# Performance work log

Measured on AMD Instinct MI355X. Metric: run time of the kernel, lower is better.

Reference implementation:

```python
import jax, jax.numpy as jnp
import numpy as np
from jax import lax

B, H, W, C = 16, 32, 32, 256
HEADS = 8
HD = C // HEADS          # attention_head_dim = 32
KSZ = 3                  # conv_kernel_size
DIL = 2                  # dilation_rate
SCALE = HD ** -0.5


def setup_inputs() -> dict:
    key = jax.random.key(0)
    k0, k1, k2, k3 = jax.random.split(key, 4)
    return {
        "query": jax.random.normal(k0, (B, H, W, C), jnp.float32),
        "key_in": jax.random.normal(k1, (B, H, W, C), jnp.float32),
        "value": jax.random.normal(k2, (B, H, W, C), jnp.float32),
        # depthwise conv: kernel [kh, kw, in_ch/groups=1, out_ch=C], plus bias [C]
        "conv_kernel": jax.random.normal(k3, (KSZ, KSZ, 1, C), jnp.float32) * 0.05,
        "conv_bias": jnp.zeros((C,), jnp.float32),
    }


def _dwconv(x, kernel, bias):
    # depthwise dilated conv, padding SAME (Keras Conv2D groups=C)
    y = lax.conv_general_dilated(
        x, kernel,
        window_strides=(1, 1), padding="SAME",
        rhs_dilation=(DIL, DIL),
        dimension_numbers=("NHWC", "HWIO", "NHWC"),
        feature_group_count=C,
    )
    return y + bias


def _to_heads(x):
    # [B,H,W,C] -> [B, heads, S, head_dim]
    return x.reshape(B, H * W, HEADS, HD).transpose(0, 2, 1, 3)


def reference(query, key_in, value, conv_kernel, conv_bias):
    q = _to_heads(query)
    k = _to_heads(_dwconv(key_in, conv_kernel, conv_bias))
    v = _to_heads(_dwconv(value, conv_kernel, conv_bias))
    scores = jnp.einsum("bhqd,bhkd->bhqk", q, k) * SCALE  # [B,heads,S,S]
    attn = jax.nn.softmax(scores, axis=-1)
    out = jnp.einsum("bhqk,bhkd->bhqd", attn, v)          # [B,heads,S,hd]
    return out.transpose(0, 2, 1, 3).reshape(B, H, W, C)
```

## Files before the change

kernel.cpp:

```cpp
#include <hip/hip_runtime.h>

#define B_    16
#define HH    32
#define WW    32
#define CC    256
#define HEADS 8
#define HD    32
#define S_    1024
#define KT    128
#define NITER (S_ / KT)
#define QF    4
#define SCALE_L2E 0.25503486f

typedef unsigned short u16;
typedef unsigned int   u32;
typedef __attribute__((ext_vector_type(8))) short short8;
typedef __attribute__((ext_vector_type(4))) float f32x4;

__device__ __forceinline__ u16 f2bf(float f) {
    u32 x = __float_as_uint(f);
    return (u16)((x + 0x7fffu + ((x >> 16) & 1u)) >> 16);
}
__device__ __forceinline__ u32 pack2bf(float lo, float hi) {
    return (u32)f2bf(lo) | ((u32)f2bf(hi) << 16);
}

#define GLD_LDS16(gp, lp)                                                 \
    __builtin_amdgcn_global_load_lds(                                     \
        (const __attribute__((address_space(1))) void*)(gp),              \
        (__attribute__((address_space(3))) void*)(lp), 16, 0, 0)

__global__ __launch_bounds__(256, 5) void dw_conv_kernel(
    const float* __restrict__ key_in, const float* __restrict__ value,
    const float* __restrict__ ck, const float* __restrict__ cb,
    u16* __restrict__ Kws, u16* __restrict__ Vws)
{
    __shared__ float4 tile[2048];

    const int tid = threadIdx.x;
    const int blk = blockIdx.x;
    const int g  = blk & 7;
    const int yt = (blk >> 3) & 7;
    const int b  = (blk >> 6) & 15;
    const int t  = blk >> 10;
    const float4* __restrict__ src4 = (const float4*)(t ? value : key_in);
    const int y0 = yt * 4;

    {
        const int x  = (tid >> 3) & 31;
        const int cc = tid & 7;
        #pragma unroll
        for (int i = 0; i < 8; i++) {
            int yy = y0 - 2 + i;
            if (yy >= 0 && yy < HH) {
                const float4* gp = src4 +
                    ((((size_t)b * HH + yy) * WW + x) * 64 + g * 8 + cc);
                GLD_LDS16(gp, &tile[tid + i * 256]);
            }
        }
    }

    const int c = tid & 7;
    float4 w9[9];
    #pragma unroll
    for (int j = 0; j < 9; j++)
        w9[j] = *(const float4*)(ck + j * CC + g * 32 + c * 4);
    const float4 bias = *(const float4*)(cb + g * 32 + c * 4);

    __syncthreads();

    #pragma unroll
    for (int i = 0; i < 4; i++) {
        int o = tid + i * 256;
        int x = (o >> 3) & 31;
        const int ry = i;
        float4 acc = bias;
        #pragma unroll
        for (int kh = 0; kh < 3; kh++) {
            int yy = y0 + ry - 2 + 2 * kh;
            if (yy < 0 || yy >= HH) continue;
            #pragma unroll
            for (int kw = 0; kw < 3; kw++) {
                int xx = x - 2 + 2 * kw;
                if (xx < 0 || xx >= WW) continue;
                float4 v = tile[((ry + 2 * kh) * 32 + xx) * 8 + c];
                float4 w = w9[kh * 3 + kw];
                acc.x += w.x * v.x; acc.y += w.y * v.y;
                acc.z += w.z * v.z; acc.w += w.w * v.w;
            }
        }
        int spix = (y0 + ry) * WW + x;
        size_t off = (((size_t)(b * HEADS + g)) * S_ + spix) * HD + c * 4;
        if (t == 0)
            *(uint2*)&Kws[off] = make_uint2(pack2bf(acc.x * SCALE_L2E, acc.y * SCALE_L2E),
                                            pack2bf(acc.z * SCALE_L2E, acc.w * SCALE_L2E));
        else
            *(uint2*)&Vws[off] = make_uint2(pack2bf(acc.x, acc.y), pack2bf(acc.z, acc.w));
    }
}

__global__ __launch_bounds__(256, 2) void attn_kernel(
    const float* __restrict__ query,
    const u16* __restrict__ Kws, const u16* __restrict__ Vws,
    float* __restrict__ out)
{
    __shared__ __align__(16) u16 Vtlds[2][HD][KT + 8];

    const int tid  = threadIdx.x;
    const int lane = tid & 63;
    const int wv   = tid >> 6;
    const int q15  = lane & 15;
    const int quad = lane >> 4;

    const int blk = blockIdx.x;
    const int bh  = blk & 127;
    const int qt  = blk >> 7;
    const int b = bh >> 3, h = bh & 7;
    const int q0w = qt * 256 + wv * 64;

    short8 qf[QF];
    #pragma unroll
    for (int f = 0; f < QF; f++) {
        const float* qp = query + ((size_t)(b * S_ + q0w + f * 16 + q15)) * CC
                          + h * HD + quad * 8;
        float4 a = *(const float4*)(qp);
        float4 c = *(const float4*)(qp + 4);
        short8 v;
        v[0] = (short)f2bf(a.x); v[1] = (short)f2bf(a.y);
        v[2] = (short)f2bf(a.z); v[3] = (short)f2bf(a.w);
        v[4] = (short)f2bf(c.x); v[5] = (short)f2bf(c.y);
        v[6] = (short)f2bf(c.z); v[7] = (short)f2bf(c.w);
        qf[f] = v;
    }

    short8 ones;
    #pragma unroll
    for (int j = 0; j < 8; j++) ones[j] = (short)0x3F80;

    const u16* Kg = Kws + (size_t)bh * S_ * HD;
    const u16* Vg = Vws + (size_t)bh * S_ * HD;

    const int vg  = tid >> 3, vs4 = tid & 7;
    const int vc = vg >> 3, vw = vg & 7;
    const int vt2 = (vw >> 2) & 1, vqd = vw & 3;
    const int vpg = (vc << 5) | (vqd << 3) | (vt2 << 2);

    uint2 vr0, vr1, vr2, vr3;

    auto issue_v_loads = [&](int kt0) {
        const uint2* vsrc = (const uint2*)(Vg + (size_t)(kt0 + 4 * vg) * HD + 4 * vs4);
        vr0 = vsrc[0]; vr1 = vsrc[8]; vr2 = vsrc[16]; vr3 = vsrc[24];
    };
    auto write_lds = [&](int p) {
        u32 a, bb;
        a  = __builtin_amdgcn_perm(vr1.x, vr0.x, 0x05040100u);
        bb = __builtin_amdgcn_perm(vr3.x, vr2.x, 0x05040100u);
        *(uint2*)&Vtlds[p][4 * vs4 + 0][vpg] = make_uint2(a, bb);
        a  = __builtin_amdgcn_perm(vr1.x, vr0.x, 0x07060302u);
        bb = __builtin_amdgcn_perm(vr3.x, vr2.x, 0x07060302u);
        *(uint2*)&Vtlds[p][4 * vs4 + 1][vpg] = make_uint2(a, bb);
        a  = __builtin_amdgcn_perm(vr1.y, vr0.y, 0x05040100u);
        bb = __builtin_amdgcn_perm(vr3.y, vr2.y, 0x05040100u);
        *(uint2*)&Vtlds[p][4 * vs4 + 2][vpg] = make_uint2(a, bb);
        a  = __builtin_amdgcn_perm(vr1.y, vr0.y, 0x07060302u);
        bb = __builtin_amdgcn_perm(vr3.y, vr2.y, 0x07060302u);
        *(uint2*)&Vtlds[p][4 * vs4 + 3][vpg] = make_uint2(a, bb);
    };

    f32x4 Ot[QF][2];
    f32x4 Dsum[QF];
    #pragma unroll
    for (int f = 0; f < QF; f++) {
        Ot[f][0] = (f32x4)0.f; Ot[f][1] = (f32x4)0.f; Dsum[f] = (f32x4)0.f;
    }

    issue_v_loads(0);
    write_lds(0);

    for (int it = 0; it < NITER; it++) {
        const int p = it & 1;
        const int kt0 = it * KT;

        short8 kfr0[4], kfr1[4];
        #pragma unroll
        for (int c = 0; c < 4; c++) {
            kfr0[c] = *(const short8*)(Kg + (size_t)(kt0 + c * 32 + q15) * HD + quad * 8);
            kfr1[c] = *(const short8*)(Kg + (size_t)(kt0 + c * 32 + 16 + q15) * HD + quad * 8);
        }
        if (it + 1 < NITER) issue_v_loads((it + 1) * KT);
        __syncthreads();

        #pragma unroll
        for (int c = 0; c < 4; c++) {
            short8 vf0 = *(const short8*)&Vtlds[p][q15][c * 32 + quad * 8];
            short8 vf1 = *(const short8*)&Vtlds[p][16 + q15][c * 32 + quad * 8];
            #pragma unroll
            for (int f = 0; f < QF; f++) {
                f32x4 s0 = __builtin_amdgcn_mfma_f32_16x16x32_bf16(kfr0[c], qf[f], (f32x4)0.f, 0, 0, 0);
                f32x4 s1 = __builtin_amdgcn_mfma_f32_16x16x32_bf16(kfr1[c], qf[f], (f32x4)0.f, 0, 0, 0);
                #pragma unroll
                for (int r = 0; r < 4; r++) {
                    s0[r] = __builtin_amdgcn_exp2f(s0[r]);
                    s1[r] = __builtin_amdgcn_exp2f(s1[r]);
                }
                union { u32 u[4]; short8 s8; } pk;
                pk.u[0] = __builtin_amdgcn_perm(__float_as_uint(s0[1]),
                                                __float_as_uint(s0[0]), 0x07060302u);
                pk.u[1] = __builtin_amdgcn_perm(__float_as_uint(s0[3]),
                                                __float_as_uint(s0[2]), 0x07060302u);
                pk.u[2] = __builtin_amdgcn_perm(__float_as_uint(s1[1]),
                                                __float_as_uint(s1[0]), 0x07060302u);
                pk.u[3] = __builtin_amdgcn_perm(__float_as_uint(s1[3]),
                                                __float_as_uint(s1[2]), 0x07060302u);
                Ot[f][0] = __builtin_amdgcn_mfma_f32_16x16x32_bf16(vf0, pk.s8, Ot[f][0], 0, 0, 0);
                Ot[f][1] = __builtin_amdgcn_mfma_f32_16x16x32_bf16(vf1, pk.s8, Ot[f][1], 0, 0, 0);
                Dsum[f]  = __builtin_amdgcn_mfma_f32_16x16x32_bf16(ones, pk.s8, Dsum[f], 0, 0, 0);
            }
        }
        if (it + 1 < NITER) write_lds((it + 1) & 1);
    }

    #pragma unroll
    for (int f = 0; f < QF; f++) {
        float inv = 1.0f / Dsum[f][0];
        int qg = q0w + f * 16 + q15;
        float* op = out + ((size_t)(b * S_ + qg)) * CC + h * HD;
        #pragma unroll
        for (int h2 = 0; h2 < 2; h2++)
            #pragma unroll
            for (int r = 0; r < 4; r++)
                op[h2 * 16 + quad * 4 + r] = Ot[f][h2][r] * inv;
    }
}

extern "C" void kernel_launch(void* const* d_in, const int* in_sizes, int n_in,
                              void* d_out, int out_size, void* d_ws, size_t ws_size,
                              hipStream_t stream)
{
    const float* query  = (const float*)d_in[0];
    const float* key_in = (const float*)d_in[1];
    const float* value  = (const float*)d_in[2];
    const float* ck     = (const float*)d_in[3];
    const float* cb     = (const float*)d_in[4];
    float* out = (float*)d_out;

    u16* Kws = (u16*)d_ws;
    u16* Vws = Kws + (size_t)B_ * HEADS * S_ * HD;

    dw_conv_kernel<<<2048, 256, 0, stream>>>(
        key_in, value, ck, cb, Kws, Vws);

    attn_kernel<<<(B_ * HEADS * S_) / 256, 256, 0, stream>>>(
        query, Kws, Vws, out);
}
```

Baseline: 124.6 us.

## Fuse depthwise conv into attention kernel with full-head K/V staged in LDS

Merges the separate depthwise-conv and attention kernels into one launch. Each 512-thread block handles one (batch, head, query-half), computes the whole dilated conv for K and V with a sliding register window down the image, and stores the bf16 K and the transposed, permuted V for all 1024 keys in shared memory. The attention loop then reads K and V from LDS with no per-iteration barriers or global traffic, and the workspace round trip is removed. In exchange, each head's conv is computed twice (once per query half), the grid shrinks to one large block per CU with about 130KB of LDS, and the conv phase is a serial per-thread loop that delays the start of the MFMA work.

```diff
diff --git a/kernel.cpp b/kernel.cpp
--- a/kernel.cpp
+++ b/kernel.cpp
@@ -25,98 +25,92 @@
     return (u32)f2bf(lo) | ((u32)f2bf(hi) << 16);
 }
 
-#define GLD_LDS16(gp, lp)                                                 \
-    __builtin_amdgcn_global_load_lds(                                     \
-        (const __attribute__((address_space(1))) void*)(gp),              \
-        (__attribute__((address_space(3))) void*)(lp), 16, 0, 0)
-
-__global__ __launch_bounds__(256, 5) void dw_conv_kernel(
+__global__ __launch_bounds__(512, 2) void fused_kernel(
+    const float* __restrict__ query,
     const float* __restrict__ key_in, const float* __restrict__ value,
     const float* __restrict__ ck, const float* __restrict__ cb,
-    u16* __restrict__ Kws, u16* __restrict__ Vws)
+    float* __restrict__ out)
 {
-    __shared__ float4 tile[2048];
-
-    const int tid = threadIdx.x;
-    const int blk = blockIdx.x;
-    const int g  = blk & 7;
-    const int yt = (blk >> 3) & 7;
-    const int b  = (blk >> 6) & 15;
-    const int t  = blk >> 10;
-    const float4* __restrict__ src4 = (const float4*)(t ? value : key_in);
-    const int y0 = yt * 4;
+    __shared__ __align__(16) u16 Klds[S_][HD];
+    __shared__ __align__(16) u16 Vt[HD][S_ + 8];
+
+    const int tid  = threadIdx.x;
+    const int blk  = blockIdx.x;
+    const int half = blk & 1;
+    const int h    = (blk >> 1) & 7;
+    const int b    = blk >> 4;
 
     {
-        const int x  = (tid >> 3) & 31;
-        const int cc = tid & 7;
-        #pragma unroll
-        for (int i = 0; i < 8; i++) {
-            int yy = y0 - 2 + i;
-            if (yy >= 0 && yy < HH) {
-                const float4* gp = src4 +
-                    ((((size_t)b * HH + yy) * WW + x) * 64 + g * 8 + cc);
-                GLD_LDS16(gp, &tile[tid + i * 256]);
+        const int t  = tid >> 8;
+        const int r8 = tid & 255;
+        const int x  = (r8 >> 3) & 31;
+        const int cq = r8 & 7;
+        const float* __restrict__ src = t ? value : key_in;
+        const size_t base = ((size_t)b * HH) * WW * CC + (size_t)h * HD + cq * 4;
+
+        float4 w9[9];
+        #pragma unroll
+        for (int j = 0; j < 9; j++)
+            w9[j] = *(const float4*)(ck + j * CC + h * HD + cq * 4);
+        const float4 bias = *(const float4*)(cb + h * HD + cq * 4);
+
+        auto tap = [&](int yy, int xx) -> float4 {
+            if (yy < 0 || yy >= HH || xx < 0 || xx >= WW)
+                return make_float4(0.f, 0.f, 0.f, 0.f);
+            return *(const float4*)(src + base + ((size_t)yy * WW + xx) * CC);
+        };
+
+        #pragma unroll
+        for (int par = 0; par < 2; par++) {
+            float4 W[3][3];
+            #pragma unroll
+            for (int kh = 0; kh < 3; kh++)
+                #pragma unroll
+                for (int kw = 0; kw < 3; kw++)
+                    W[kh][kw] = tap(par - 2 + 2 * kh, x - 2 + 2 * kw);
+            #pragma unroll
+            for (int y = par; y < HH; y += 2) {
+                float4 acc = bias;
+                #pragma unroll
+                for (int kh = 0; kh < 3; kh++)
+                    #pragma unroll
+                    for (int kw = 0; kw < 3; kw++) {
+                        float4 v = W[kh][kw], w = w9[kh * 3 + kw];
+                        acc.x += w.x * v.x; acc.y += w.y * v.y;
+                        acc.z += w.z * v.z; acc.w += w.w * v.w;
+                    }
+                const int pix = y * WW + x;
+                if (t == 0) {
+                    *(uint2*)&Klds[pix][cq * 4] =
+                        make_uint2(pack2bf(acc.x * SCALE_L2E, acc.y * SCALE_L2E),
+                                   pack2bf(acc.z * SCALE_L2E, acc.w * SCALE_L2E));
+                } else {
+                    const int k5  = pix & 31;
+                    const int col = (pix & ~31) | ((k5 & 12) << 1)
+                                  | ((k5 & 16) >> 2) | (k5 & 3);
+                    Vt[cq * 4 + 0][col] = f2bf(acc.x);
+                    Vt[cq * 4 + 1][col] = f2bf(acc.y);
+                    Vt[cq * 4 + 2][col] = f2bf(acc.z);
+                    Vt[cq * 4 + 3][col] = f2bf(acc.w);
+                }
+                #pragma unroll
+                for (int kh = 0; kh < 2; kh++)
+                    #pragma unroll
+                    for (int kw = 0; kw < 3; kw++)
+                        W[kh][kw] = W[kh + 1][kw];
+                #pragma unroll
+                for (int kw = 0; kw < 3; kw++)
+                    W[2][kw] = tap(y + 4, x - 2 + 2 * kw);
             }
         }
     }
-
-    const int c = tid & 7;
-    float4 w9[9];
-    #pragma unroll
-    for (int j = 0; j < 9; j++)
-        w9[j] = *(const float4*)(ck + j * CC + g * 32 + c * 4);
-    const float4 bias = *(const float4*)(cb + g * 32 + c * 4);
-
     __syncthreads();
 
-    #pragma unroll
-    for (int i = 0; i < 4; i++) {
-        int o = tid + i * 256;
-        int x = (o >> 3) & 31;
-        const int ry = i;
-        float4 acc = bias;
-        #pragma unroll
-        for (int kh = 0; kh < 3; kh++) {
-            int yy = y0 + ry - 2 + 2 * kh;
-            if (yy < 0 || yy >= HH) continue;
-            #pragma unroll
-            for (int kw = 0; kw < 3; kw++) {
-                int xx = x - 2 + 2 * kw;
-                if (xx < 0 || xx >= WW) continue;
-                float4 v = tile[((ry + 2 * kh) * 32 + xx) * 8 + c];
-                float4 w = w9[kh * 3 + kw];
-                acc.x += w.x * v.x; acc.y += w.y * v.y;
-                acc.z += w.z * v.z; acc.w += w.w * v.w;
-            }
-        }
-        int spix = (y0 + ry) * WW + x;
-        size_t off = (((size_t)(b * HEADS + g)) * S_ + spix) * HD + c * 4;
-        if (t == 0)
-            *(uint2*)&Kws[off] = make_uint2(pack2bf(acc.x * SCALE_L2E, acc.y * SCALE_L2E),
-                                            pack2bf(acc.z * SCALE_L2E, acc.w * SCALE_L2E));
-        else
-            *(uint2*)&Vws[off] = make_uint2(pack2bf(acc.x, acc.y), pack2bf(acc.z, acc.w));
-    }
-}
-
-__global__ __launch_bounds__(256, 2) void attn_kernel(
-    const float* __restrict__ query,
-    const u16* __restrict__ Kws, const u16* __restrict__ Vws,
-    float* __restrict__ out)
-{
-    __shared__ __align__(16) u16 Vtlds[2][HD][KT + 8];
-
-    const int tid  = threadIdx.x;
     const int lane = tid & 63;
     const int wv   = tid >> 6;
     const int q15  = lane & 15;
     const int quad = lane >> 4;
-
-    const int blk = blockIdx.x;
-    const int bh  = blk & 127;
-    const int qt  = blk >> 7;
-    const int b = bh >> 3, h = bh & 7;
-    const int q0w = qt * 256 + wv * 64;
+    const int q0w  = half * 512 + wv * 64;
 
     short8 qf[QF];
     #pragma unroll
@@ -137,36 +131,6 @@
     #pragma unroll
     for (int j = 0; j < 8; j++) ones[j] = (short)0x3F80;
 
-    const u16* Kg = Kws + (size_t)bh * S_ * HD;
-    const u16* Vg = Vws + (size_t)bh * S_ * HD;
-
-    const int vg  = tid >> 3, vs4 = tid & 7;
-    const int vc = vg >> 3, vw = vg & 7;
-    const int vt2 = (vw >> 2) & 1, vqd = vw & 3;
-    const int vpg = (vc << 5) | (vqd << 3) | (vt2 << 2);
-
-    uint2 vr0, vr1, vr2, vr3;
-
-    auto issue_v_loads = [&](int kt0) {
-        const uint2* vsrc = (const uint2*)(Vg + (size_t)(kt0 + 4 * vg) * HD + 4 * vs4);
-        vr0 = vsrc[0]; vr1 = vsrc[8]; vr2 = vsrc[16]; vr3 = vsrc[24];
-    };
-    auto write_lds = [&](int p) {
-        u32 a, bb;
-        a  = __builtin_amdgcn_perm(vr1.x, vr0.x, 0x05040100u);
-        bb = __builtin_amdgcn_perm(vr3.x, vr2.x, 0x05040100u);
-        *(uint2*)&Vtlds[p][4 * vs4 + 0][vpg] = make_uint2(a, bb);
-        a  = __builtin_amdgcn_perm(vr1.x, vr0.x, 0x07060302u);
-        bb = __builtin_amdgcn_perm(vr3.x, vr2.x, 0x07060302u);
-        *(uint2*)&Vtlds[p][4 * vs4 + 1][vpg] = make_uint2(a, bb);
-        a  = __builtin_amdgcn_perm(vr1.y, vr0.y, 0x05040100u);
-        bb = __builtin_amdgcn_perm(vr3.y, vr2.y, 0x05040100u);
-        *(uint2*)&Vtlds[p][4 * vs4 + 2][vpg] = make_uint2(a, bb);
-        a  = __builtin_amdgcn_perm(vr1.y, vr0.y, 0x07060302u);
-        bb = __builtin_amdgcn_perm(vr3.y, vr2.y, 0x07060302u);
-        *(uint2*)&Vtlds[p][4 * vs4 + 3][vpg] = make_uint2(a, bb);
-    };
-
     f32x4 Ot[QF][2];
     f32x4 Dsum[QF];
     #pragma unroll
@@ -174,26 +138,20 @@
         Ot[f][0] = (f32x4)0.f; Ot[f][1] = (f32x4)0.f; Dsum[f] = (f32x4)0.f;
     }
 
-    issue_v_loads(0);
-    write_lds(0);
-
     for (int it = 0; it < NITER; it++) {
-        const int p = it & 1;
         const int kt0 = it * KT;
 
         short8 kfr0[4], kfr1[4];
         #pragma unroll
         for (int c = 0; c < 4; c++) {
-            kfr0[c] = *(const short8*)(Kg + (size_t)(kt0 + c * 32 + q15) * HD + quad * 8);
-            kfr1[c] = *(const short8*)(Kg + (size_t)(kt0 + c * 32 + 16 + q15) * HD + quad * 8);
+            kfr0[c] = *(const short8*)&Klds[kt0 + c * 32 + q15][quad * 8];
+            kfr1[c] = *(const short8*)&Klds[kt0 + c * 32 + 16 + q15][quad * 8];
         }
-        if (it + 1 < NITER) issue_v_loads((it + 1) * KT);
-        __syncthreads();
 
         #pragma unroll
         for (int c = 0; c < 4; c++) {
-            short8 vf0 = *(const short8*)&Vtlds[p][q15][c * 32 + quad * 8];
-            short8 vf1 = *(const short8*)&Vtlds[p][16 + q15][c * 32 + quad * 8];
+            short8 vf0 = *(const short8*)&Vt[q15][kt0 + c * 32 + quad * 8];
+            short8 vf1 = *(const short8*)&Vt[16 + q15][kt0 + c * 32 + quad * 8];
             #pragma unroll
             for (int f = 0; f < QF; f++) {
                 f32x4 s0 = __builtin_amdgcn_mfma_f32_16x16x32_bf16(kfr0[c], qf[f], (f32x4)0.f, 0, 0, 0);
@@ -217,7 +175,6 @@
                 Dsum[f]  = __builtin_amdgcn_mfma_f32_16x16x32_bf16(ones, pk.s8, Dsum[f], 0, 0, 0);
             }
         }
-        if (it + 1 < NITER) write_lds((it + 1) & 1);
     }
 
     #pragma unroll
@@ -243,13 +200,8 @@
     const float* ck     = (const float*)d_in[3];
     const float* cb     = (const float*)d_in[4];
     float* out = (float*)d_out;
-
-    u16* Kws = (u16*)d_ws;
-    u16* Vws = Kws + (size_t)B_ * HEADS * S_ * HD;
-
-    dw_conv_kernel<<<2048, 256, 0, stream>>>(
-        key_in, value, ck, cb, Kws, Vws);
-
-    attn_kernel<<<(B_ * HEADS * S_) / 256, 256, 0, stream>>>(
-        query, Kws, Vws, out);
-}
+    (void)d_ws; (void)ws_size;
+
+    fused_kernel<<<B_ * HEADS * 2, 512, 0, stream>>>(
+        query, key_in, value, ck, cb, out);
+}
```

Result: slower. 129.7 us (+4.1%).
